# Optimization experiments

Measured on AMD Instinct MI355X. Metric: run time of the kernel, lower is better.

Reference implementation:

```python
import jax, jax.numpy as jnp
from jax import lax
import numpy as np

B, CIN, T, H, W = 32, 512, 16, 7, 7
A = 9                 # 3 scales x 3 ratios
STRIDE = 16.0
NMS_THRESH = 0.7      # cfg.TEST.RPN_NMS_THRESH
POST_NMS = 300        # cfg.TEST.RPN_POST_NMS_TOP_N


def _gen_anchors():
    # faithful port of generate_anchors(base_size=16, ratios=[0.5,1,2], scales=[4,8,16])
    base = 16.0
    ratios = np.array([0.5, 1.0, 2.0])
    scales = np.array([4.0, 8.0, 16.0])
    ctr = (base - 1.0) / 2.0
    size = base * base
    ws = np.round(np.sqrt(size / ratios))
    hs = np.round(ws * ratios)
    def mk(ws, hs, xc, yc):
        return np.stack([xc - 0.5 * (ws - 1), yc - 0.5 * (hs - 1),
                         xc + 0.5 * (ws - 1), yc + 0.5 * (hs - 1)], 1)
    ratio_anchors = mk(ws, hs, ctr, ctr)            # [3,4]
    outs = []
    for a in ratio_anchors:                         # scale enum per ratio anchor
        w = a[2] - a[0] + 1.0
        h = a[3] - a[1] + 1.0
        xc = a[0] + 0.5 * (w - 1)
        yc = a[1] + 0.5 * (h - 1)
        outs.append(mk(w * scales, h * scales, xc, yc))
    return np.concatenate(outs, 0).astype(np.float32)  # [9,4]


def _shifted_anchors():
    sx = (np.arange(W) * STRIDE).astype(np.float32)
    sy = (np.arange(H) * STRIDE).astype(np.float32)
    mx, my = np.meshgrid(sx, sy)                    # x fastest, matches HWA flatten
    shifts = np.stack([mx.ravel(), my.ravel(), mx.ravel(), my.ravel()], 1)  # [K,4]
    return (shifts[:, None, :] + _gen_anchors()[None, :, :]).reshape(-1, 4)  # [K*A,4]

_ALL_ANCHORS = jnp.asarray(_shifted_anchors())      # [441,4]


def conv3d(x, w, b, pad):
    y = lax.conv_general_dilated(x, w, (1, 1, 1),
                                 [(pad[0], pad[0]), (pad[1], pad[1]), (pad[2], pad[2])],
                                 dimension_numbers=('NCDHW', 'OIDHW', 'NCDHW'))
    return y + b[None, :, None, None, None]


def conv1x1(x, w, b):
    return jnp.einsum('bchw,oc->bohw', x, w[:, :, 0, 0]) + b[None, :, None, None]


def softmax_2way(score):
    # reshape(x,2) -> softmax over dim 1 -> reshape back (fg/bg pairwise softmax)
    b, c, h, w = score.shape
    s = score.reshape(b, 2, (c // 2) * h, w)
    return jax.nn.softmax(s, axis=1).reshape(b, c, h, w)


def bbox_decode(anchors, deltas):
    # anchors [N,4], deltas [B,N,4] -> boxes [B,N,4] (bbox_transform_inv)
    w = anchors[:, 2] - anchors[:, 0] + 1.0
    h = anchors[:, 3] - anchors[:, 1] + 1.0
    cx = anchors[:, 0] + 0.5 * w
    cy = anchors[:, 1] + 0.5 * h
    pcx = deltas[..., 0] * w + cx
    pcy = deltas[..., 1] * h + cy
    pw = jnp.exp(deltas[..., 2]) * w
    ph = jnp.exp(deltas[..., 3]) * h
    return jnp.stack([pcx - 0.5 * pw, pcy - 0.5 * ph,
                      pcx + 0.5 * pw, pcy + 0.5 * ph], axis=-1)


def clip_boxes(boxes, info):
    # boxes [N,4], info = (im_h, im_w, scale)
    x1 = jnp.clip(boxes[:, 0], 0.0, info[1] - 1.0)
    y1 = jnp.clip(boxes[:, 1], 0.0, info[0] - 1.0)
    x2 = jnp.clip(boxes[:, 2], 0.0, info[1] - 1.0)
    y2 = jnp.clip(boxes[:, 3], 0.0, info[0] - 1.0)
    return jnp.stack([x1, y1, x2, y2], 1)


def nms_single(boxes, scores):
    # greedy NMS, fixed shapes: boxes [N,4] -> kept boxes padded to [POST_NMS,4]
    order = jnp.argsort(-scores)
    b = boxes[order]
    n = b.shape[0]
    areas = (b[:, 2] - b[:, 0] + 1.0) * (b[:, 3] - b[:, 1] + 1.0)
    idx = jnp.arange(n)
    def body(i, keep):
        xx1 = jnp.maximum(b[i, 0], b[:, 0])
        yy1 = jnp.maximum(b[i, 1], b[:, 1])
        xx2 = jnp.minimum(b[i, 2], b[:, 2])
        yy2 = jnp.minimum(b[i, 3], b[:, 3])
        inter = jnp.clip(xx2 - xx1 + 1.0, 0.0) * jnp.clip(yy2 - yy1 + 1.0, 0.0)
        iou = inter / (areas[i] + areas - inter)
        sup = (idx > i) & (iou > NMS_THRESH) & keep[i]
        return keep & ~sup
    keep = lax.fori_loop(0, n, body, jnp.ones((n,), bool))
    sel = jnp.sort(jnp.where(keep, idx, n))[:POST_NMS]
    valid = sel < n
    selc = jnp.minimum(sel, n - 1)
    return jnp.where(valid[:, None], b[selc], 0.0)


def proposal_layer(cls_prob, bbox_pred, im_info):
    b = cls_prob.shape[0]
    scores = cls_prob[:, A:, :, :].transpose(0, 2, 3, 1).reshape(b, -1)   # fg scores [B,K*A]
    deltas = bbox_pred.transpose(0, 2, 3, 1).reshape(b, -1, 4)
    props = bbox_decode(_ALL_ANCHORS, deltas)
    props = jax.vmap(clip_boxes)(props, im_info)
    boxes = jax.vmap(nms_single)(props, scores)                           # [B,POST_NMS,4]
    bidx = jnp.broadcast_to(jnp.arange(b, dtype=boxes.dtype)[:, None, None],
                            (b, POST_NMS, 1))
    return jnp.concatenate([bidx, boxes], axis=2)                         # [B,POST_NMS,5]


def setup_inputs() -> dict:
    key = jax.random.key(0)
    ks = jax.random.split(key, 8)
    s = 0.05
    return {
        'base_feat': jax.random.normal(ks[0], (B, CIN, T, H, W), jnp.float32),
        'im_info': jnp.tile(jnp.array([[112.0, 112.0, 1.0]], jnp.float32), (B, 1)),
        'gt_boxes': jnp.zeros((B, 1, 7), jnp.float32),
        'num_boxes': jnp.zeros((B,), jnp.int32),
        'rpn_conv_w': jax.random.normal(ks[1], (512, CIN, 3, 3, 3), jnp.float32) * s,
        'rpn_conv_b': jnp.zeros((512,), jnp.float32),
        't16_w': jax.random.normal(ks[2], (512, 512, 16, 3, 3), jnp.float32) * s,
        't16_b': jnp.zeros((512,), jnp.float32),
        'cls_w': jax.random.normal(ks[3], (2 * A, 512, 1, 1), jnp.float32) * s,
        'cls_b': jnp.zeros((2 * A,), jnp.float32),
        'bbox_w': jax.random.normal(ks[4], (4 * A, 512, 1, 1), jnp.float32) * s,
        'bbox_b': jnp.zeros((4 * A,), jnp.float32),
    }


def reference(base_feat, im_info, gt_boxes, num_boxes,
              rpn_conv_w, rpn_conv_b, t16_w, t16_b,
              cls_w, cls_b, bbox_w, bbox_b):
    x = jax.nn.relu(conv3d(base_feat, rpn_conv_w, rpn_conv_b, (1, 1, 1)))     # [B,512,16,7,7]
    f16 = jax.nn.relu(conv3d(x, t16_w, t16_b, (0, 1, 1)))                     # [B,512,1,7,7]
    f16 = f16.transpose(0, 2, 1, 3, 4).reshape(-1, 512, H, W)                 # [B,512,7,7]
    cls_score = conv1x1(f16, cls_w, cls_b)                                    # [B,18,7,7]
    cls_prob = softmax_2way(cls_score)
    bbox_pred = conv1x1(f16, bbox_w, bbox_b)                                  # [B,36,7,7]
    # proposals use .data in the original -> detached
    rois = proposal_layer(lax.stop_gradient(cls_prob),
                          lax.stop_gradient(bbox_pred), im_info)
    return rois, cls_prob, bbox_pred
```

## Files before the change

### kernel.cpp

```cpp
#include <hip/hip_runtime.h>
#include <hip/hip_bf16.h>
#include <cmath>

typedef __bf16 bf16_t;
typedef unsigned short u16;
typedef unsigned int u32;
typedef float f32x4 __attribute__((ext_vector_type(4)));
typedef short s16x8 __attribute__((ext_vector_type(8)));
typedef u32   u32x4 __attribute__((ext_vector_type(4)));
#define DEVINL __device__ __forceinline__
#define POSTN 300

#define XPT_OFF  0ull
#define YTL_OFF  11943936ull
#define YT_OFF   23887872ull
#define F_OFF    45121536ull
#define PART_OFF 48332800ull
#define SC_OFF   51544064ull
#define BX_OFF   51600512ull
#define K1_OFF   51826304ull
#define K2_OFF   51881600ull
#define FLAG_OFF 52176512ull
#define NEED     52176516ull

DEVINL float ldf(const void* p, long i, int f32m) {
  return f32m ? ((const float*)p)[i] : (float)(((const bf16_t*)p)[i]);
}

DEVINL float clampf(float v, float lo, float hi) {
  if (!(v == v)) return lo;
  if (v < lo) return lo;
  if (v > hi) return hi;
  return v;
}

DEVINL void split3(float v, u16& hb, u16& mb, u16& lb) {
  bf16_t h = (bf16_t)v; float fh = (float)h;
  float r1 = v - fh;
  bf16_t m = (bf16_t)r1; float fm_ = (float)m;
  float r2 = r1 - fm_;
  bf16_t l = (bf16_t)r2;
  __builtin_memcpy(&hb, &h, 2);
  __builtin_memcpy(&mb, &m, 2);
  __builtin_memcpy(&lb, &l, 2);
}

__global__ __launch_bounds__(256) void detect_dtype(const void* bf, const void* w1, int* flag) {
  __shared__ int cnt;
  int tid = threadIdx.x;
  if (tid == 0) cnt = 0;
  __syncthreads();
  float a = (float)(((const bf16_t*)bf)[2 * tid]);
  float b = (float)(((const bf16_t*)w1)[2 * tid]);
  int wc = 0;
  if (!(a == a) || fabsf(a) > 1e20f || (a != 0.f && fabsf(a) < 1e-20f)) wc++;
  if (!(b == b) || fabsf(b) > 1e20f || (b != 0.f && fabsf(b) < 1e-20f)) wc++;
  atomicAdd(&cnt, wc);
  __syncthreads();
  if (tid == 0) *flag = (cnt >= 16) ? 1 : 0;
}

__global__ __launch_bounds__(256) void build_koff(int* k1, int* k2) {
  int i = blockIdx.x * 256 + threadIdx.x;
  if (i < 13824) {
    int ci = i / 27, tap = i % 27;
    k1[i] = ci * 1458 + (tap / 9) * 81 + ((tap % 9) / 3) * 9 + (tap % 3);
  }
  if (i < 73728) {
    int ci = i / 144, tap = i % 144;
    k2[i] = ci * 1296 + (tap / 9) * 81 + ((tap % 9) / 3) * 9 + (tap % 3);
  }
}

__global__ __launch_bounds__(256) void pad_x(const void* __restrict__ X,
                                             float* __restrict__ XpT, u16* __restrict__ Xp16,
                                             const int* __restrict__ flagp, int cb) {
  int f32m = *flagp;
  long e = (long)blockIdx.x * 256 + threadIdx.x;
  if (e >= 8L * 512 * 784) return;
  int f = (int)(e % 784);
  long bc = e / 784;
  int t = f / 49, h = (f % 49) / 7, w = f % 7;
  long src = (long)cb * 512 * 784 + bc * 784 + f;
  long idx = bc * 1458 + (t + 1) * 81 + (h + 1) * 9 + (w + 1);
  if (f32m) XpT[idx] = ((const float*)X)[src];
  else      Xp16[idx] = ((const u16*)X)[src];
}

template <int MODE>
__global__ __launch_bounds__(256) void gemm_f32(
    const float* __restrict__ Act, const void* __restrict__ Wgt, const void* __restrict__ bias,
    float* __restrict__ Yt, float* __restrict__ Part,
    const int* __restrict__ koff, const int* __restrict__ flagp) {
  const int f32m = *flagp;
  if (f32m == 0) return;
  const int tid = threadIdx.x;
  int mt, nt, s = 0;
  if (MODE == 1) { mt = blockIdx.x % 98; nt = blockIdx.x / 98; }
  else           { mt = blockIdx.x % 7;  nt = (blockIdx.x / 7) % 8; s = blockIdx.x / 56; }
  const int m0 = mt * 64, n0 = nt * 64;
  const int K     = (MODE == 1) ? 13824 : 18432;
  const int kBase = (MODE == 1) ? 0     : s * 18432;
  const int WROW  = (MODE == 1) ? 13824 : 73728;

  __shared__ __align__(16) float As[64][68];
  __shared__ __align__(16) float Bs[64][68];

  const int am = tid & 63, akq = tid >> 6;
  long aBase;
  {
    int m = m0 + am;
    if (MODE == 1) {
      int b = m / 784, r = m % 784, t = r / 49, h = (r % 49) / 7, w = r % 7;
      aBase = (long)b * (512 * 1458) + t * 81 + h * 9 + w;
    } else {
      if (m > 391) m = 391;
      int b = m / 49, r = m % 49, h = r / 7, w = r % 7;
      aBase = (long)b * (512 * 1296) + h * 9 + w;
    }
  }
  const int bn = tid >> 2, bks = (tid & 3) * 16;
  const long bBase = (long)(n0 + bn) * WROW + kBase;

  float acc[4][4] = {{0.f}};
  const int tx = tid & 15, ty = tid >> 4;

  for (int k0 = 0; k0 < K; k0 += 64) {
    __syncthreads();
#pragma unroll
    for (int j = 0; j < 16; j++) {
      int kk = akq * 16 + j;
      As[kk][am] = Act[aBase + koff[kBase + k0 + kk]];
    }
#pragma unroll
    for (int j = 0; j < 16; j++) {
      int kk = bks + j;
      Bs[kk][bn] = ldf(Wgt, bBase + k0 + kk, f32m);
    }
    __syncthreads();
#pragma unroll 8
    for (int k = 0; k < 64; k++) {
      f32x4 a = *(const f32x4*)&As[k][tx * 4];
      f32x4 b = *(const f32x4*)&Bs[k][ty * 4];
#pragma unroll
      for (int i = 0; i < 4; i++)
#pragma unroll
        for (int j = 0; j < 4; j++) acc[i][j] += a[i] * b[j];
    }
  }

#pragma unroll
  for (int i = 0; i < 4; i++) {
    int m = m0 + tx * 4 + i;
#pragma unroll
    for (int j = 0; j < 4; j++) {
      int n = n0 + ty * 4 + j;
      if (MODE == 1) {
        int b = m / 784, r = m % 784, t = r / 49, h = (r % 49) / 7, w = r % 7;
        float v = acc[i][j] + ldf(bias, n, f32m);
        v = fmaxf(v, 0.f);
        Yt[(long)(b * 512 + n) * 1296 + t * 81 + (h + 1) * 9 + (w + 1)] = v;
      } else {
        if (m < 392) Part[((long)s * 392 + m) * 512 + n] = acc[i][j];
      }
    }
  }
}

__global__ __launch_bounds__(256) void gemm_mf1(
    const u16* __restrict__ Act16, const void* __restrict__ Wgt, const void* __restrict__ bias,
    u32* __restrict__ YtHM, u16* __restrict__ YtL,
    const int* __restrict__ koff, const int* __restrict__ flagp) {
  if (*flagp != 0) return;
  const int tid = threadIdx.x;
  const int mt = blockIdx.x % 49, nt = blockIdx.x / 49;
  const int m0 = mt * 128, n0 = nt * 64;

  __shared__ u16 As[128 * 64];
  __shared__ u16 Bs[64 * 64];

  const int am = tid & 127, khu = tid >> 7;
  long aBase;
  {
    int m = m0 + am;
    int b = m / 784, r = m % 784, t = r / 49, h = (r % 49) / 7, w = r % 7;
    aBase = (long)b * (512 * 1458) + t * 81 + h * 9 + w;
  }
  const u16* __restrict__ Ap = Act16 + aBase;
  const int awb = am * 64, asw = (am & 7) << 3;

  const int bn = tid & 63, bq = tid >> 6;
  const u16* __restrict__ Bp = (const u16*)Wgt + (long)(n0 + bn) * 13824;
  const int bwb = bn * 64, bsw = (bn & 7) << 3;

  const int lane = tid & 63, wv = tid >> 6;
  const int wm = (wv & 1) * 64, wn = (wv >> 1) * 32;
  const int lr = lane & 15, lq = lane >> 4;

  f32x4 acc[4][2];
#pragma unroll
  for (int i = 0; i < 4; ++i)
#pragma unroll
    for (int j = 0; j < 2; ++j) acc[i][j] = f32x4{0.f, 0.f, 0.f, 0.f};

  for (int k0 = 0; k0 < 13824; k0 += 64) {
    __syncthreads();
#pragma unroll
    for (int j = 0; j < 4; ++j) {
      const int o = k0 + khu * 32 + j * 8;
      const u16 e0 = Ap[koff[o + 0]], e1 = Ap[koff[o + 1]];
      const u16 e2 = Ap[koff[o + 2]], e3 = Ap[koff[o + 3]];
      const u16 e4 = Ap[koff[o + 4]], e5 = Ap[koff[o + 5]];
      const u16 e6 = Ap[koff[o + 6]], e7 = Ap[koff[o + 7]];
      u32x4 V = { (u32)e0 | ((u32)e1 << 16), (u32)e2 | ((u32)e3 << 16),
                  (u32)e4 | ((u32)e5 << 16), (u32)e6 | ((u32)e7 << 16) };
      *(u32x4*)&As[awb + ((khu * 32 + j * 8) ^ asw)] = V;
    }
    {
      const u32x4* wp = (const u32x4*)(Bp + k0 + bq * 16);
      *(u32x4*)&Bs[bwb + ((bq * 16) ^ bsw)] = wp[0];
      *(u32x4*)&Bs[bwb + ((bq * 16 + 8) ^ bsw)] = wp[1];
    }
    __syncthreads();
#pragma unroll
    for (int kk = 0; kk < 64; kk += 32) {
      const int kf = kk + lq * 8;
      s16x8 a[4], b[2];
#pragma unroll
      for (int fm = 0; fm < 4; ++fm) {
        const int row = wm + fm * 16 + lr;
        a[fm] = *(const s16x8*)&As[row * 64 + (kf ^ ((lr & 7) << 3))];
      }
#pragma unroll
      for (int fn = 0; fn < 2; ++fn) {
        const int row = wn + fn * 16 + lr;
        b[fn] = *(const s16x8*)&Bs[row * 64 + (kf ^ ((lr & 7) << 3))];
      }
#pragma unroll
      for (int fm = 0; fm < 4; ++fm)
#pragma unroll
        for (int fn = 0; fn < 2; ++fn)
          acc[fm][fn] = __builtin_amdgcn_mfma_f32_16x16x32_bf16(a[fm], b[fn], acc[fm][fn], 0, 0, 0);
    }
  }

#pragma unroll
  for (int fn = 0; fn < 2; ++fn) {
    const int n = n0 + wn + fn * 16 + lr;
    const float bv = (float)(((const bf16_t*)bias)[n]);
#pragma unroll
    for (int fm = 0; fm < 4; ++fm)
#pragma unroll
      for (int r = 0; r < 4; ++r) {
        const int m = m0 + wm + fm * 16 + lq * 4 + r;
        int b = m / 784, rr = m % 784, t = rr / 49, hh = (rr % 49) / 7, ww = rr % 7;
        float v = fmaxf(acc[fm][fn][r] + bv, 0.f);
        u16 hb, mb, lb; split3(v, hb, mb, lb);
        long idx = (long)(b * 512 + n) * 1296 + t * 81 + (hh + 1) * 9 + (ww + 1);
        YtHM[idx] = ((u32)hb << 16) | mb;
        YtL[idx] = lb;
      }
  }
}

__global__ __launch_bounds__(256) void gemm_mf2(
    const u32* __restrict__ AHM, const u16* __restrict__ AL, const void* __restrict__ Wgt,
    float* __restrict__ Part, const int* __restrict__ koff, const int* __restrict__ flagp) {
  if (*flagp != 0) return;
  const int tid = threadIdx.x;
  const int mt = blockIdx.x % 7, nt = (blockIdx.x / 7) % 8, s = blockIdx.x / 56;
  const int m0 = mt * 64, n0 = nt * 64;
  const int kBase = s * 18432;

  __shared__ u16 AsH[64 * 64], AsM[64 * 64], AsL[64 * 64];
  __shared__ u16 Bs[64 * 64];

  const int am = tid & 63, kq = tid >> 6;
  long aBase;
  {
    int m = m0 + am; if (m > 391) m = 391;
    int b = m / 49, r = m % 49, h = r / 7, w = r % 7;
    aBase = (long)b * (512 * 1296) + h * 9 + w;
  }
  const u32* __restrict__ ApHM = AHM + aBase;
  const u16* __restrict__ ApL  = AL + aBase;
  const int awb = am * 64, asw = (am & 7) << 3;

  const int bn = tid & 63, bq = tid >> 6;
  const u16* __restrict__ Bp = (const u16*)Wgt + (long)(n0 + bn) * 73728 + kBase;
  const int bwb = bn * 64, bsw = (bn & 7) << 3;

  const int lane = tid & 63, wv = tid >> 6;
  const int wm = (wv & 1) * 32, wn = (wv >> 1) * 32;
  const int lr = lane & 15, lq = lane >> 4;

  f32x4 acc[2][2];
#pragma unroll
  for (int i = 0; i < 2; ++i)
#pragma unroll
    for (int j = 0; j < 2; ++j) acc[i][j] = f32x4{0.f, 0.f, 0.f, 0.f};

  for (int k0 = 0; k0 < 18432; k0 += 64) {
    __syncthreads();
#pragma unroll
    for (int g = 0; g < 2; ++g) {
      const int o = kBase + k0 + kq * 16 + g * 8;
      const int i0 = koff[o + 0], i1 = koff[o + 1], i2 = koff[o + 2], i3 = koff[o + 3],
                i4 = koff[o + 4], i5 = koff[o + 5], i6 = koff[o + 6], i7 = koff[o + 7];
      const u32 q0 = ApHM[i0], q1 = ApHM[i1], q2 = ApHM[i2], q3 = ApHM[i3],
                q4 = ApHM[i4], q5 = ApHM[i5], q6 = ApHM[i6], q7 = ApHM[i7];
      const int wi = awb + ((kq * 16 + g * 8) ^ asw);
      u32x4 H = { (q0 >> 16) | (q1 & 0xffff0000u), (q2 >> 16) | (q3 & 0xffff0000u),
                  (q4 >> 16) | (q5 & 0xffff0000u), (q6 >> 16) | (q7 & 0xffff0000u) };
      *(u32x4*)&AsH[wi] = H;
      u32x4 M = { (q0 & 0xffffu) | (q1 << 16), (q2 & 0xffffu) | (q3 << 16),
                  (q4 & 0xffffu) | (q5 << 16), (q6 & 0xffffu) | (q7 << 16) };
      *(u32x4*)&AsM[wi] = M;
      u32x4 L = { (u32)ApL[i0] | ((u32)ApL[i1] << 16), (u32)ApL[i2] | ((u32)ApL[i3] << 16),
                  (u32)ApL[i4] | ((u32)ApL[i5] << 16), (u32)ApL[i6] | ((u32)ApL[i7] << 16) };
      *(u32x4*)&AsL[wi] = L;
    }
    {
      const u32x4* wp = (const u32x4*)(Bp + k0 + bq * 16);
      *(u32x4*)&Bs[bwb + ((bq * 16) ^ bsw)] = wp[0];
      *(u32x4*)&Bs[bwb + ((bq * 16 + 8) ^ bsw)] = wp[1];
    }
    __syncthreads();
#pragma unroll
    for (int kk = 0; kk < 64; kk += 32) {
      const int kf = kk + lq * 8;
      s16x8 ah[2], am_[2], al[2], b[2];
#pragma unroll
      for (int fm = 0; fm < 2; ++fm) {
        const int off = (wm + fm * 16 + lr) * 64 + (kf ^ ((lr & 7) << 3));
        ah[fm] = *(const s16x8*)&AsH[off];
        am_[fm] = *(const s16x8*)&AsM[off];
        al[fm] = *(const s16x8*)&AsL[off];
      }
#pragma unroll
      for (int fn = 0; fn < 2; ++fn) {
        const int off = (wn + fn * 16 + lr) * 64 + (kf ^ ((lr & 7) << 3));
        b[fn] = *(const s16x8*)&Bs[off];
      }
#pragma unroll
      for (int fm = 0; fm < 2; ++fm)
#pragma unroll
        for (int fn = 0; fn < 2; ++fn) {
          acc[fm][fn] = __builtin_amdgcn_mfma_f32_16x16x32_bf16(ah[fm], b[fn], acc[fm][fn], 0, 0, 0);
          acc[fm][fn] = __builtin_amdgcn_mfma_f32_16x16x32_bf16(am_[fm], b[fn], acc[fm][fn], 0, 0, 0);
          acc[fm][fn] = __builtin_amdgcn_mfma_f32_16x16x32_bf16(al[fm], b[fn], acc[fm][fn], 0, 0, 0);
        }
    }
  }

#pragma unroll
  for (int fn = 0; fn < 2; ++fn) {
    const int n = n0 + wn + fn * 16 + lr;
#pragma unroll
    for (int fm = 0; fm < 2; ++fm)
#pragma unroll
      for (int r = 0; r < 4; ++r) {
        const int m = m0 + wm + fm * 16 + lq * 4 + r;
        if (m < 392) Part[((long)s * 392 + m) * 512 + n] = acc[fm][fn][r];
      }
  }
}

__global__ __launch_bounds__(256) void reduce2(const float* __restrict__ Part,
                                               const void* __restrict__ bias,
                                               float* __restrict__ F,
                                               const int* __restrict__ flagp, int chunk) {
  int f32m = *flagp;
  int idx = blockIdx.x * 256 + threadIdx.x;
  if (idx >= 392 * 512) return;
  int m = idx >> 9, n = idx & 511;
  float v = 0.f;
  for (int s = 0; s < 4; s++) v += Part[((long)s * 392 + m) * 512 + n];
  v += ldf(bias, n, f32m);
  F[((long)chunk * 392 + m) * 512 + n] = fmaxf(v, 0.f);
}

__global__ __launch_bounds__(256) void heads(
    const float* __restrict__ F, const void* __restrict__ cls_w, const void* __restrict__ cls_b,
    const void* __restrict__ bbox_w, const void* __restrict__ bbox_b,
    const void* __restrict__ im_info, float* __restrict__ out_cls, float* __restrict__ out_bbox,
    float* __restrict__ scores, float* __restrict__ boxes, const int* __restrict__ flagp) {
  int f32m = *flagp;
  int m = blockIdx.x;
  int bg = m / 49, r2 = m % 49, h = r2 / 7, w = r2 % 7;
  __shared__ float Fr[512];
  __shared__ float partial[256];
  __shared__ float outv[54];
  int tid = threadIdx.x;
  Fr[tid] = F[(long)m * 512 + tid];
  Fr[tid + 256] = F[(long)m * 512 + tid + 256];
  __syncthreads();
  int o = tid & 63, ch = tid >> 6;
  float p = 0.f;
  if (o < 54) {
    const void* wp = (o < 18) ? cls_w : bbox_w;
    long wrow = (o < 18) ? (long)o * 512 : (long)(o - 18) * 512;
    int c0 = ch * 128;
    for (int c = c0; c < c0 + 128; c++) p += Fr[c] * ldf(wp, wrow + c, f32m);
  }
  partial[tid] = p;
  __syncthreads();
  if (tid < 54) {
    float v = partial[tid] + partial[tid + 64] + partial[tid + 128] + partial[tid + 192];
    v += (tid < 18) ? ldf(cls_b, tid, f32m) : ldf(bbox_b, tid - 18, f32m);
    outv[tid] = v;
  }
  __syncthreads();
  if (tid < 18) {
    int a = tid % 9;
    float s0 = outv[a], s1 = outv[a + 9];
    float mx = fmaxf(s0, s1);
    float e0 = expf(s0 - mx), e1 = expf(s1 - mx);
    float pr = ((tid < 9) ? e0 : e1) / (e0 + e1);
    if (!(pr == pr)) pr = 0.f;
    out_cls[(((long)(bg * 18 + tid)) * 7 + h) * 7 + w] = pr;
    if (tid >= 9) scores[bg * 441 + (h * 7 + w) * 9 + a] = pr;
  } else if (tid < 54) {
    float v = outv[tid];
    if (!(v == v)) v = 0.f;
    out_bbox[(((long)(bg * 36 + (tid - 18))) * 7 + h) * 7 + w] = v;
  } else if (tid < 63) {
    int a = tid - 54;
    int ridx = a / 3, sidx = a % 3;
    float ratio = (ridx == 0) ? 0.5f : ((ridx == 1) ? 1.f : 2.f);
    float scale = (sidx == 0) ? 4.f : ((sidx == 1) ? 8.f : 16.f);
    float ws0 = rintf(sqrtf(256.f / ratio));
    float hs0 = rintf(ws0 * ratio);
    float x1 = 7.5f - 0.5f * (ws0 - 1.f), y1 = 7.5f - 0.5f * (hs0 - 1.f);
    float x2 = 7.5f + 0.5f * (ws0 - 1.f), y2 = 7.5f + 0.5f * (hs0 - 1.f);
    float w_ = x2 - x1 + 1.f, h_ = y2 - y1 + 1.f;
    float xc = x1 + 0.5f * (w_ - 1.f), yc = y1 + 0.5f * (h_ - 1.f);
    float ws2 = w_ * scale, hs2 = h_ * scale;
    float ax1 = xc - 0.5f * (ws2 - 1.f) + w * 16.f;
    float ay1 = yc - 0.5f * (hs2 - 1.f) + h * 16.f;
    float ax2 = xc + 0.5f * (ws2 - 1.f) + w * 16.f;
    float ay2 = yc + 0.5f * (hs2 - 1.f) + h * 16.f;
    float wA = ax2 - ax1 + 1.f, hA = ay2 - ay1 + 1.f;
    float cxA = ax1 + 0.5f * wA, cyA = ay1 + 0.5f * hA;
    float d0 = outv[18 + 4 * a], d1 = outv[19 + 4 * a];
    float d2 = outv[20 + 4 * a], d3 = outv[21 + 4 * a];
    float pcx = d0 * wA + cxA, pcy = d1 * hA + cyA;
    float pw = expf(d2) * wA, ph = expf(d3) * hA;
    float iw = ldf(im_info, bg * 3 + 1, f32m) - 1.f;
    float ih = ldf(im_info, bg * 3 + 0, f32m) - 1.f;
    float bx1 = clampf(pcx - 0.5f * pw, 0.f, iw);
    float by1 = clampf(pcy - 0.5f * ph, 0.f, ih);
    float bx2 = clampf(pcx + 0.5f * pw, 0.f, iw);
    float by2 = clampf(pcy + 0.5f * ph, 0.f, ih);
    int ai = bg * 441 + (h * 7 + w) * 9 + a;
    boxes[ai * 4 + 0] = bx1; boxes[ai * 4 + 1] = by1;
    boxes[ai * 4 + 2] = bx2; boxes[ai * 4 + 3] = by2;
  }
}

__global__ __launch_bounds__(256) void nms_kernel(const float* __restrict__ scores,
                                                  const float* __restrict__ boxes,
                                                  float* __restrict__ rois) {
  int bg = blockIdx.x;
  int tid = threadIdx.x;
  __shared__ float rsc[441];
  __shared__ unsigned short ord[441];
  __shared__ float sbx[441][4];
  __shared__ float sar[441];
  __shared__ unsigned long long sup[441][8];
  __shared__ unsigned long long kw[8];
  for (int i = tid; i < 441; i += 256) { rsc[i] = scores[bg * 441 + i]; ord[i] = (unsigned short)i; }
  if (tid < 8) kw[tid] = 0ull;
  __syncthreads();
  for (int i = tid; i < 441; i += 256) {
    float si = rsc[i];
    int rk = 0;
    for (int j = 0; j < 441; j++) {
      float sj = rsc[j];
      rk += (sj > si) || (sj == si && j < i);
    }
    if (rk < 441) ord[rk] = (unsigned short)i;
  }
  __syncthreads();
  for (int r = tid; r < 441; r += 256) {
    int i = ord[r];
    float x1 = boxes[(bg * 441 + i) * 4 + 0], y1 = boxes[(bg * 441 + i) * 4 + 1];
    float x2 = boxes[(bg * 441 + i) * 4 + 2], y2 = boxes[(bg * 441 + i) * 4 + 3];
    sbx[r][0] = x1; sbx[r][1] = y1; sbx[r][2] = x2; sbx[r][3] = y2;
    sar[r] = (x2 - x1 + 1.f) * (y2 - y1 + 1.f);
  }
  __syncthreads();
  for (int task = tid; task < 441 * 7; task += 256) {
    int r = task / 7, wd = task % 7;
    float x1 = sbx[r][0], y1 = sbx[r][1], x2 = sbx[r][2], y2 = sbx[r][3];
    float ar = sar[r];
    unsigned long long msk = 0ull;
    int jbase = wd * 64;
    for (int bit = 0; bit < 64; bit++) {
      int j = jbase + bit;
      if (j > r && j < 441) {
        float xx1 = fmaxf(x1, sbx[j][0]);
        float yy1 = fmaxf(y1, sbx[j][1]);
        float xx2 = fminf(x2, sbx[j][2]);
        float yy2 = fminf(y2, sbx[j][3]);
        float iwv = fmaxf(xx2 - xx1 + 1.f, 0.f);
        float ihv = fmaxf(yy2 - yy1 + 1.f, 0.f);
        float inter = iwv * ihv;
        float iou = inter / (ar + sar[j] - inter);
        if (iou > 0.7f) msk |= (1ull << bit);
      }
    }
    sup[r][wd] = msk;
  }
  __syncthreads();
  if (tid < 64) {
    int wd = (tid < 7) ? tid : 7;
    unsigned long long rmw = 0ull;
    for (int i = 0; i < 441; i++) {
      int ow = i >> 6, obit = i & 63;
      int mykeep = ((rmw >> obit) & 1ull) ? 0 : 1;
      int kept = __shfl(mykeep, ow, 64);
      if (kept && wd < 7) rmw |= sup[i][wd];
    }
    if (wd < 7) {
      unsigned long long k = ~rmw;
      if (wd == 6) k &= (1ull << 57) - 1;
      kw[wd] = k;
    }
  }
  __syncthreads();
  for (int r = tid; r < POSTN; r += 256) {
    long oo = ((long)bg * POSTN + r) * 5;
    rois[oo] = (float)bg;
    rois[oo + 1] = 0.f; rois[oo + 2] = 0.f;
    rois[oo + 3] = 0.f; rois[oo + 4] = 0.f;
  }
  __syncthreads();
  for (int r = tid; r < 441; r += 256) {
    int wd = r >> 6, bit = r & 63;
    if ((kw[wd] >> bit) & 1ull) {
      int slot = 0;
      for (int q = 0; q < wd; q++) slot += __popcll(kw[q]);
      slot += __popcll(kw[wd] & ((1ull << bit) - 1ull));
      if (slot < POSTN) {
        long oo = ((long)bg * POSTN + slot) * 5;
        rois[oo + 1] = sbx[r][0];
        rois[oo + 2] = sbx[r][1];
        rois[oo + 3] = sbx[r][2];
        rois[oo + 4] = sbx[r][3];
      }
    }
  }
}

__global__ __launch_bounds__(256) void scrub_f32(float* __restrict__ o, int n) {
  int i = blockIdx.x * 256 + threadIdx.x;
  if (i >= n) return;
  float v = o[i];
  if (!(v == v) || fabsf(v) > 1e30f) o[i] = 0.f;
}

__global__ __launch_bounds__(256) void fallback_out(float* __restrict__ out, int total) {
  int i = blockIdx.x * 256 + threadIdx.x;
  if (i >= total) return;
  out[i] = 0.f;
}

extern "C" void kernel_launch(void* const* d_in, const int* in_sizes, int n_in,
                              void* d_out, int out_size, void* d_ws, size_t ws_size,
                              hipStream_t stream) {
  const void* base_feat = d_in[0];
  const void* im_info   = d_in[1];
  const void* w1 = d_in[4];
  const void* b1 = d_in[5];
  const void* w2 = d_in[6];
  const void* b2 = d_in[7];
  const void* cw = d_in[8];
  const void* cb = d_in[9];
  const void* bw = d_in[10];
  const void* bb = d_in[11];
  float* out = (float*)d_out;

  if (ws_size < NEED) {
    fallback_out<<<(out_size + 255) / 256, 256, 0, stream>>>(out, out_size);
    return;
  }

  char* ws = (char*)d_ws;
  float* XpT  = (float*)(ws + XPT_OFF);
  u16*   Xp16 = (u16*)(ws + XPT_OFF);
  u16*   YtL  = (u16*)(ws + YTL_OFF);
  float* Yt   = (float*)(ws + YT_OFF);
  u32*   YtHM = (u32*)(ws + YT_OFF);
  float* F    = (float*)(ws + F_OFF);
  float* Part = (float*)(ws + PART_OFF);
  float* Sc   = (float*)(ws + SC_OFF);
  float* Bx   = (float*)(ws + BX_OFF);
  int*   K1   = (int*)(ws + K1_OFF);
  int*   K2   = (int*)(ws + K2_OFF);
  int*   Flag = (int*)(ws + FLAG_OFF);

  detect_dtype<<<1, 256, 0, stream>>>(base_feat, w1, Flag);
  build_koff<<<288, 256, 0, stream>>>(K1, K2);

  for (int c = 0; c < 4; c++) {
    hipMemsetAsync(XpT, 0, 23887872ull, stream);
    hipMemsetAsync(Yt, 0, 21233664ull, stream);
    pad_x<<<12544, 256, 0, stream>>>(base_feat, XpT, Xp16, Flag, c * 8);
    gemm_f32<1><<<784, 256, 0, stream>>>(XpT, w1, b1, Yt, nullptr, K1, Flag);
    gemm_mf1<<<392, 256, 0, stream>>>(Xp16, w1, b1, YtHM, YtL, K1, Flag);
    gemm_f32<2><<<224, 256, 0, stream>>>(Yt, w2, nullptr, nullptr, Part, K2, Flag);
    gemm_mf2<<<224, 256, 0, stream>>>(YtHM, YtL, w2, Part, K2, Flag);
    reduce2<<<784, 256, 0, stream>>>(Part, b2, F, Flag, c);
  }

  heads<<<1568, 256, 0, stream>>>(F, cw, cb, bw, bb, im_info,
                                  out + 48000, out + 76224, Sc, Bx, Flag);
  nms_kernel<<<32, 256, 0, stream>>>(Sc, Bx, out);
  scrub_f32<<<(out_size + 255) / 256, 256, 0, stream>>>(out, out_size);
}
```

Baseline: 10.35 ms.

## Use channel-last padded input and pre-transposed weights for bf16 conv GEMM

For the bf16 path the padded input is now stored channel-innermost, and conv1 weights are pre-transposed to tap-major order. The first GEMM can then load activation tiles with contiguous 16-byte vector reads per tap instead of gathering scalars through an offset table. The intermediate hi/mid and low split parts are packed into one 8-byte element so the second GEMM does a single gather per element. Batch chunks shrink from 8 to 4 images over 8 iterations, with more K-splits in GEMM2, and the per-chunk memsets are replaced by one memset plus pad kernels that write zeros themselves. Tile counts change, and more kernel launches are traded for smaller working sets.

```diff
diff --git a/kernel.cpp b/kernel.cpp
--- a/kernel.cpp
+++ b/kernel.cpp
@@ -7,12 +7,15 @@
 typedef unsigned int u32;
 typedef float f32x4 __attribute__((ext_vector_type(4)));
 typedef short s16x8 __attribute__((ext_vector_type(8)));
+typedef u32   u32x2 __attribute__((ext_vector_type(2)));
 typedef u32   u32x4 __attribute__((ext_vector_type(4)));
 #define DEVINL __device__ __forceinline__
 #define POSTN 300
 
 #define XPT_OFF  0ull
-#define YTL_OFF  11943936ull
+#define XP16_OFF 0ull
+#define W1T_OFF  5971968ull
+#define YTP_OFF  20127744ull
 #define YT_OFF   23887872ull
 #define F_OFF    45121536ull
 #define PART_OFF 48332800ull
@@ -72,19 +75,58 @@
   }
 }
 
-__global__ __launch_bounds__(256) void pad_x(const void* __restrict__ X,
-                                             float* __restrict__ XpT, u16* __restrict__ Xp16,
-                                             const int* __restrict__ flagp, int cb) {
-  int f32m = *flagp;
-  long e = (long)blockIdx.x * 256 + threadIdx.x;
-  if (e >= 8L * 512 * 784) return;
-  int f = (int)(e % 784);
-  long bc = e / 784;
-  int t = f / 49, h = (f % 49) / 7, w = f % 7;
-  long src = (long)cb * 512 * 784 + bc * 784 + f;
-  long idx = bc * 1458 + (t + 1) * 81 + (h + 1) * 9 + (w + 1);
-  if (f32m) XpT[idx] = ((const float*)X)[src];
-  else      Xp16[idx] = ((const u16*)X)[src];
+__global__ __launch_bounds__(256) void build_w1t(const void* __restrict__ w1,
+                                                 u16* __restrict__ w1T,
+                                                 const int* __restrict__ flagp) {
+  if (*flagp != 0) return;
+  int id = blockIdx.x * 256 + threadIdx.x;
+  if (id >= 512 * 27 * 64) return;
+  int co = id / 1728, r = id % 1728, tap = r / 64, cio = r % 64;
+  const u16* W = (const u16*)w1;
+  u16 t[8];
+#pragma unroll
+  for (int e = 0; e < 8; e++) t[e] = W[co * 13824 + (cio * 8 + e) * 27 + tap];
+  u32x4 v = { (u32)t[0] | ((u32)t[1] << 16), (u32)t[2] | ((u32)t[3] << 16),
+              (u32)t[4] | ((u32)t[5] << 16), (u32)t[6] | ((u32)t[7] << 16) };
+  *(u32x4*)&w1T[co * 13824 + tap * 512 + cio * 8] = v;
+}
+
+__global__ __launch_bounds__(256) void pad_f32(const void* __restrict__ X,
+                                               float* __restrict__ XpT,
+                                               const int* __restrict__ flagp, int cb) {
+  if (*flagp == 0) return;
+  int e = blockIdx.x * 256 + threadIdx.x;
+  if (e >= 4 * 512 * 1458) return;
+  int bc = e / 1458, p = e % 1458;
+  int tp = p / 81, hp = (p % 81) / 9, wp = p % 9;
+  float v = 0.f;
+  if (tp >= 1 && tp < 17 && hp >= 1 && hp < 8 && wp >= 1 && wp < 8) {
+    int f = (tp - 1) * 49 + (hp - 1) * 7 + (wp - 1);
+    v = ((const float*)X)[((long)cb * 512 + bc) * 784 + f];
+  }
+  XpT[e] = v;
+}
+
+__global__ __launch_bounds__(256) void pad_b16(const void* __restrict__ X,
+                                               u16* __restrict__ Xp16,
+                                               const int* __restrict__ flagp, int cb) {
+  if (*flagp != 0) return;
+  int id = blockIdx.x * 256 + threadIdx.x;
+  if (id >= 5832 * 64) return;
+  int pos = id >> 6, cio = id & 63;
+  int b = pos / 1458, r = pos % 1458;
+  int tp = r / 81, hp = (r % 81) / 9, wp = r % 9;
+  u16 t[8] = {0, 0, 0, 0, 0, 0, 0, 0};
+  if (tp >= 1 && tp < 17 && hp >= 1 && hp < 8 && wp >= 1 && wp < 8) {
+    int f = (tp - 1) * 49 + (hp - 1) * 7 + (wp - 1);
+    const u16* Xs = (const u16*)X;
+#pragma unroll
+    for (int e = 0; e < 8; e++)
+      t[e] = Xs[((long)(cb + b) * 512 + cio * 8 + e) * 784 + f];
+  }
+  u32x4 v = { (u32)t[0] | ((u32)t[1] << 16), (u32)t[2] | ((u32)t[3] << 16),
+              (u32)t[4] | ((u32)t[5] << 16), (u32)t[6] | ((u32)t[7] << 16) };
+  *(u32x4*)&Xp16[(long)pos * 512 + cio * 8] = v;
 }
 
 template <int MODE>
@@ -96,12 +138,13 @@
   if (f32m == 0) return;
   const int tid = threadIdx.x;
   int mt, nt, s = 0;
-  if (MODE == 1) { mt = blockIdx.x % 98; nt = blockIdx.x / 98; }
-  else           { mt = blockIdx.x % 7;  nt = (blockIdx.x / 7) % 8; s = blockIdx.x / 56; }
+  if (MODE == 1) { mt = blockIdx.x % 49; nt = blockIdx.x / 49; }
+  else           { mt = blockIdx.x & 3;  nt = (blockIdx.x >> 2) & 7; s = blockIdx.x >> 5; }
   const int m0 = mt * 64, n0 = nt * 64;
-  const int K     = (MODE == 1) ? 13824 : 18432;
-  const int kBase = (MODE == 1) ? 0     : s * 18432;
+  const int K     = (MODE == 1) ? 13824 : 9216;
+  const int kBase = (MODE == 1) ? 0     : s * 9216;
   const int WROW  = (MODE == 1) ? 13824 : 73728;
+  const int MTOT  = (MODE == 1) ? 3136  : 196;
 
   __shared__ __align__(16) float As[64][68];
   __shared__ __align__(16) float Bs[64][68];
@@ -109,12 +152,11 @@
   const int am = tid & 63, akq = tid >> 6;
   long aBase;
   {
-    int m = m0 + am;
+    int m = m0 + am; if (m > MTOT - 1) m = MTOT - 1;
     if (MODE == 1) {
       int b = m / 784, r = m % 784, t = r / 49, h = (r % 49) / 7, w = r % 7;
       aBase = (long)b * (512 * 1458) + t * 81 + h * 9 + w;
     } else {
-      if (m > 391) m = 391;
       int b = m / 49, r = m % 49, h = r / 7, w = r % 7;
       aBase = (long)b * (512 * 1296) + h * 9 + w;
     }
@@ -161,36 +203,33 @@
         v = fmaxf(v, 0.f);
         Yt[(long)(b * 512 + n) * 1296 + t * 81 + (h + 1) * 9 + (w + 1)] = v;
       } else {
-        if (m < 392) Part[((long)s * 392 + m) * 512 + n] = acc[i][j];
+        if (m < 196) Part[((long)s * 196 + m) * 512 + n] = acc[i][j];
       }
     }
   }
 }
 
 __global__ __launch_bounds__(256) void gemm_mf1(
-    const u16* __restrict__ Act16, const void* __restrict__ Wgt, const void* __restrict__ bias,
-    u32* __restrict__ YtHM, u16* __restrict__ YtL,
-    const int* __restrict__ koff, const int* __restrict__ flagp) {
+    const u16* __restrict__ Xp16, const u16* __restrict__ w1T, const void* __restrict__ bias,
+    u32x2* __restrict__ YtP, const int* __restrict__ flagp) {
   if (*flagp != 0) return;
   const int tid = threadIdx.x;
-  const int mt = blockIdx.x % 49, nt = blockIdx.x / 49;
+  const int mt = blockIdx.x % 25, nt = blockIdx.x / 25;
   const int m0 = mt * 128, n0 = nt * 64;
 
   __shared__ u16 As[128 * 64];
   __shared__ u16 Bs[64 * 64];
 
-  const int am = tid & 127, khu = tid >> 7;
-  long aBase;
-  {
-    int m = m0 + am;
+  int rowbase[4];
+#pragma unroll
+  for (int i = 0; i < 4; ++i) {
+    int id = tid + 256 * i;
+    int m = m0 + (id >> 3); if (m > 3135) m = 3135;
     int b = m / 784, r = m % 784, t = r / 49, h = (r % 49) / 7, w = r % 7;
-    aBase = (long)b * (512 * 1458) + t * 81 + h * 9 + w;
-  }
-  const u16* __restrict__ Ap = Act16 + aBase;
-  const int awb = am * 64, asw = (am & 7) << 3;
-
+    rowbase[i] = ((((b * 18) + (t + 1)) * 9 + (h + 1)) * 9 + (w + 1)) * 512;
+  }
   const int bn = tid & 63, bq = tid >> 6;
-  const u16* __restrict__ Bp = (const u16*)Wgt + (long)(n0 + bn) * 13824;
+  const u16* __restrict__ Bp = w1T + (long)(n0 + bn) * 13824;
   const int bwb = bn * 64, bsw = (bn & 7) << 3;
 
   const int lane = tid & 63, wv = tid >> 6;
@@ -203,44 +242,50 @@
 #pragma unroll
     for (int j = 0; j < 2; ++j) acc[i][j] = f32x4{0.f, 0.f, 0.f, 0.f};
 
-  for (int k0 = 0; k0 < 13824; k0 += 64) {
-    __syncthreads();
-#pragma unroll
-    for (int j = 0; j < 4; ++j) {
-      const int o = k0 + khu * 32 + j * 8;
-      const u16 e0 = Ap[koff[o + 0]], e1 = Ap[koff[o + 1]];
-      const u16 e2 = Ap[koff[o + 2]], e3 = Ap[koff[o + 3]];
-      const u16 e4 = Ap[koff[o + 4]], e5 = Ap[koff[o + 5]];
-      const u16 e6 = Ap[koff[o + 6]], e7 = Ap[koff[o + 7]];
-      u32x4 V = { (u32)e0 | ((u32)e1 << 16), (u32)e2 | ((u32)e3 << 16),
-                  (u32)e4 | ((u32)e5 << 16), (u32)e6 | ((u32)e7 << 16) };
-      *(u32x4*)&As[awb + ((khu * 32 + j * 8) ^ asw)] = V;
-    }
-    {
-      const u32x4* wp = (const u32x4*)(Bp + k0 + bq * 16);
-      *(u32x4*)&Bs[bwb + ((bq * 16) ^ bsw)] = wp[0];
-      *(u32x4*)&Bs[bwb + ((bq * 16 + 8) ^ bsw)] = wp[1];
-    }
-    __syncthreads();
-#pragma unroll
-    for (int kk = 0; kk < 64; kk += 32) {
-      const int kf = kk + lq * 8;
-      s16x8 a[4], b[2];
-#pragma unroll
-      for (int fm = 0; fm < 4; ++fm) {
-        const int row = wm + fm * 16 + lr;
-        a[fm] = *(const s16x8*)&As[row * 64 + (kf ^ ((lr & 7) << 3))];
-      }
-#pragma unroll
-      for (int fn = 0; fn < 2; ++fn) {
-        const int row = wn + fn * 16 + lr;
-        b[fn] = *(const s16x8*)&Bs[row * 64 + (kf ^ ((lr & 7) << 3))];
-      }
-#pragma unroll
-      for (int fm = 0; fm < 4; ++fm)
-#pragma unroll
-        for (int fn = 0; fn < 2; ++fn)
-          acc[fm][fn] = __builtin_amdgcn_mfma_f32_16x16x32_bf16(a[fm], b[fn], acc[fm][fn], 0, 0, 0);
+  for (int tap = 0; tap < 27; ++tap) {
+    const int dt = tap / 9, dh = (tap % 9) / 3, dw = tap % 3;
+    const int tapshift = dt * 41472 + dh * 4608 + dw * 512;
+    for (int cib = 0; cib < 8; ++cib) {
+      const int off = tapshift + cib * 64;
+      __syncthreads();
+      u32x4 va[4];
+#pragma unroll
+      for (int i = 0; i < 4; ++i) {
+        int id = tid + 256 * i;
+        va[i] = *(const u32x4*)&Xp16[rowbase[i] + off + (id & 7) * 8];
+      }
+#pragma unroll
+      for (int i = 0; i < 4; ++i) {
+        int id = tid + 256 * i;
+        int row = id >> 3, oct = id & 7;
+        *(u32x4*)&As[row * 64 + ((oct * 8) ^ ((row & 7) << 3))] = va[i];
+      }
+      {
+        const u32x4* wp = (const u32x4*)(Bp + tap * 512 + cib * 64 + bq * 16);
+        *(u32x4*)&Bs[bwb + ((bq * 16) ^ bsw)] = wp[0];
+        *(u32x4*)&Bs[bwb + ((bq * 16 + 8) ^ bsw)] = wp[1];
+      }
+      __syncthreads();
+#pragma unroll
+      for (int kk = 0; kk < 64; kk += 32) {
+        const int kf = kk + lq * 8;
+        s16x8 a[4], b[2];
+#pragma unroll
+        for (int fm = 0; fm < 4; ++fm) {
+          const int row = wm + fm * 16 + lr;
+          a[fm] = *(const s16x8*)&As[row * 64 + (kf ^ ((lr & 7) << 3))];
+        }
+#pragma unroll
+        for (int fn = 0; fn < 2; ++fn) {
+          const int row = wn + fn * 16 + lr;
+          b[fn] = *(const s16x8*)&Bs[row * 64 + (kf ^ ((lr & 7) << 3))];
+        }
+#pragma unroll
+        for (int fm = 0; fm < 4; ++fm)
+#pragma unroll
+          for (int fn = 0; fn < 2; ++fn)
+            acc[fm][fn] = __builtin_amdgcn_mfma_f32_16x16x32_bf16(a[fm], b[fn], acc[fm][fn], 0, 0, 0);
+      }
     }
   }
 
@@ -253,24 +298,25 @@
 #pragma unroll
       for (int r = 0; r < 4; ++r) {
         const int m = m0 + wm + fm * 16 + lq * 4 + r;
-        int b = m / 784, rr = m % 784, t = rr / 49, hh = (rr % 49) / 7, ww = rr % 7;
-        float v = fmaxf(acc[fm][fn][r] + bv, 0.f);
-        u16 hb, mb, lb; split3(v, hb, mb, lb);
-        long idx = (long)(b * 512 + n) * 1296 + t * 81 + (hh + 1) * 9 + (ww + 1);
-        YtHM[idx] = ((u32)hb << 16) | mb;
-        YtL[idx] = lb;
+        if (m < 3136) {
+          int b = m / 784, rr = m % 784, t = rr / 49, hh = (rr % 49) / 7, ww = rr % 7;
+          float v = fmaxf(acc[fm][fn][r] + bv, 0.f);
+          u16 hb, mb, lb; split3(v, hb, mb, lb);
+          long idx = (long)(b * 512 + n) * 1296 + t * 81 + (hh + 1) * 9 + (ww + 1);
+          YtP[idx] = u32x2{ ((u32)hb << 16) | mb, (u32)lb };
+        }
       }
   }
 }
 
 __global__ __launch_bounds__(256) void gemm_mf2(
-    const u32* __restrict__ AHM, const u16* __restrict__ AL, const void* __restrict__ Wgt,
+    const u32x2* __restrict__ AP, const void* __restrict__ Wgt,
     float* __restrict__ Part, const int* __restrict__ koff, const int* __restrict__ flagp) {
   if (*flagp != 0) return;
   const int tid = threadIdx.x;
-  const int mt = blockIdx.x % 7, nt = (blockIdx.x / 7) % 8, s = blockIdx.x / 56;
+  const int mt = blockIdx.x & 3, nt = (blockIdx.x >> 2) & 7, s = blockIdx.x >> 5;
   const int m0 = mt * 64, n0 = nt * 64;
-  const int kBase = s * 18432;
+  const int kBase = s * 9216;
 
   __shared__ u16 AsH[64 * 64], AsM[64 * 64], AsL[64 * 64];
   __shared__ u16 Bs[64 * 64];
@@ -278,12 +324,11 @@
   const int am = tid & 63, kq = tid >> 6;
   long aBase;
   {
-    int m = m0 + am; if (m > 391) m = 391;
+    int m = m0 + am; if (m > 195) m = 195;
     int b = m / 49, r = m % 49, h = r / 7, w = r % 7;
     aBase = (long)b * (512 * 1296) + h * 9 + w;
   }
-  const u32* __restrict__ ApHM = AHM + aBase;
-  const u16* __restrict__ ApL  = AL + aBase;
+  const u32x2* __restrict__ Ap = AP + aBase;
   const int awb = am * 64, asw = (am & 7) << 3;
 
   const int bn = tid & 63, bq = tid >> 6;
@@ -300,24 +345,24 @@
 #pragma unroll
     for (int j = 0; j < 2; ++j) acc[i][j] = f32x4{0.f, 0.f, 0.f, 0.f};
 
-  for (int k0 = 0; k0 < 18432; k0 += 64) {
+  for (int k0 = 0; k0 < 9216; k0 += 64) {
     __syncthreads();
 #pragma unroll
     for (int g = 0; g < 2; ++g) {
       const int o = kBase + k0 + kq * 16 + g * 8;
       const int i0 = koff[o + 0], i1 = koff[o + 1], i2 = koff[o + 2], i3 = koff[o + 3],
                 i4 = koff[o + 4], i5 = koff[o + 5], i6 = koff[o + 6], i7 = koff[o + 7];
-      const u32 q0 = ApHM[i0], q1 = ApHM[i1], q2 = ApHM[i2], q3 = ApHM[i3],
-                q4 = ApHM[i4], q5 = ApHM[i5], q6 = ApHM[i6], q7 = ApHM[i7];
+      const u32x2 q0 = Ap[i0], q1 = Ap[i1], q2 = Ap[i2], q3 = Ap[i3],
+                  q4 = Ap[i4], q5 = Ap[i5], q6 = Ap[i6], q7 = Ap[i7];
       const int wi = awb + ((kq * 16 + g * 8) ^ asw);
-      u32x4 H = { (q0 >> 16) | (q1 & 0xffff0000u), (q2 >> 16) | (q3 & 0xffff0000u),
-                  (q4 >> 16) | (q5 & 0xffff0000u), (q6 >> 16) | (q7 & 0xffff0000u) };
+      u32x4 H = { (q0.x >> 16) | (q1.x & 0xffff0000u), (q2.x >> 16) | (q3.x & 0xffff0000u),
+                  (q4.x >> 16) | (q5.x & 0xffff0000u), (q6.x >> 16) | (q7.x & 0xffff0000u) };
       *(u32x4*)&AsH[wi] = H;
-      u32x4 M = { (q0 & 0xffffu) | (q1 << 16), (q2 & 0xffffu) | (q3 << 16),
-                  (q4 & 0xffffu) | (q5 << 16), (q6 & 0xffffu) | (q7 << 16) };
+      u32x4 M = { (q0.x & 0xffffu) | (q1.x << 16), (q2.x & 0xffffu) | (q3.x << 16),
+                  (q4.x & 0xffffu) | (q5.x << 16), (q6.x & 0xffffu) | (q7.x << 16) };
       *(u32x4*)&AsM[wi] = M;
-      u32x4 L = { (u32)ApL[i0] | ((u32)ApL[i1] << 16), (u32)ApL[i2] | ((u32)ApL[i3] << 16),
-                  (u32)ApL[i4] | ((u32)ApL[i5] << 16), (u32)ApL[i6] | ((u32)ApL[i7] << 16) };
+      u32x4 L = { q0.y | (q1.y << 16), q2.y | (q3.y << 16),
+                  q4.y | (q5.y << 16), q6.y | (q7.y << 16) };
       *(u32x4*)&AsL[wi] = L;
     }
     {
@@ -361,7 +406,7 @@
 #pragma unroll
       for (int r = 0; r < 4; ++r) {
         const int m = m0 + wm + fm * 16 + lq * 4 + r;
-        if (m < 392) Part[((long)s * 392 + m) * 512 + n] = acc[fm][fn][r];
+        if (m < 196) Part[((long)s * 196 + m) * 512 + n] = acc[fm][fn][r];
       }
   }
 }
@@ -372,12 +417,13 @@
                                                const int* __restrict__ flagp, int chunk) {
   int f32m = *flagp;
   int idx = blockIdx.x * 256 + threadIdx.x;
-  if (idx >= 392 * 512) return;
+  if (idx >= 196 * 512) return;
   int m = idx >> 9, n = idx & 511;
   float v = 0.f;
-  for (int s = 0; s < 4; s++) v += Part[((long)s * 392 + m) * 512 + n];
+#pragma unroll
+  for (int s = 0; s < 8; s++) v += Part[((long)s * 196 + m) * 512 + n];
   v += ldf(bias, n, f32m);
-  F[((long)chunk * 392 + m) * 512 + n] = fmaxf(v, 0.f);
+  F[((long)chunk * 196 + m) * 512 + n] = fmaxf(v, 0.f);
 }
 
 __global__ __launch_bounds__(256) void heads(
@@ -588,10 +634,10 @@
 
   char* ws = (char*)d_ws;
   float* XpT  = (float*)(ws + XPT_OFF);
-  u16*   Xp16 = (u16*)(ws + XPT_OFF);
-  u16*   YtL  = (u16*)(ws + YTL_OFF);
+  u16*   Xp16 = (u16*)(ws + XP16_OFF);
+  u16*   W1T  = (u16*)(ws + W1T_OFF);
+  u32x2* YtP  = (u32x2*)(ws + YTP_OFF);
   float* Yt   = (float*)(ws + YT_OFF);
-  u32*   YtHM = (u32*)(ws + YT_OFF);
   float* F    = (float*)(ws + F_OFF);
   float* Part = (float*)(ws + PART_OFF);
   float* Sc   = (float*)(ws + SC_OFF);
@@ -602,16 +648,17 @@
 
   detect_dtype<<<1, 256, 0, stream>>>(base_feat, w1, Flag);
   build_koff<<<288, 256, 0, stream>>>(K1, K2);
-
-  for (int c = 0; c < 4; c++) {
-    hipMemsetAsync(XpT, 0, 23887872ull, stream);
-    hipMemsetAsync(Yt, 0, 21233664ull, stream);
-    pad_x<<<12544, 256, 0, stream>>>(base_feat, XpT, Xp16, Flag, c * 8);
-    gemm_f32<1><<<784, 256, 0, stream>>>(XpT, w1, b1, Yt, nullptr, K1, Flag);
-    gemm_mf1<<<392, 256, 0, stream>>>(Xp16, w1, b1, YtHM, YtL, K1, Flag);
-    gemm_f32<2><<<224, 256, 0, stream>>>(Yt, w2, nullptr, nullptr, Part, K2, Flag);
-    gemm_mf2<<<224, 256, 0, stream>>>(YtHM, YtL, w2, Part, K2, Flag);
-    reduce2<<<784, 256, 0, stream>>>(Part, b2, F, Flag, c);
+  build_w1t<<<3456, 256, 0, stream>>>(w1, W1T, Flag);
+  hipMemsetAsync(ws + YTP_OFF, 0, 45121536ull - YTP_OFF, stream);
+
+  for (int c = 0; c < 8; c++) {
+    pad_f32<<<11664, 256, 0, stream>>>(base_feat, XpT, Flag, c * 4);
+    pad_b16<<<1458, 256, 0, stream>>>(base_feat, Xp16, Flag, c * 4);
+    gemm_f32<1><<<392, 256, 0, stream>>>(XpT, w1, b1, Yt, nullptr, K1, Flag);
+    gemm_mf1<<<200, 256, 0, stream>>>(Xp16, W1T, b1, YtP, Flag);
+    gemm_f32<2><<<256, 256, 0, stream>>>(Yt, w2, nullptr, nullptr, Part, K2, Flag);
+    gemm_mf2<<<256, 256, 0, stream>>>(YtP, w2, Part, K2, Flag);
+    reduce2<<<392, 256, 0, stream>>>(Part, b2, F, Flag, c);
   }
 
   heads<<<1568, 256, 0, stream>>>(F, cw, cb, bw, bb, im_info,
```

New measurement: 11.56 ms. 1.12x slower.
